# Performance work log

Measured on AMD Instinct MI355X. Metric: run time of the kernel, lower is better.

Reference implementation:

```python
import jax, jax.numpy as jnp
import numpy as np

DIM = 1024
NUM_HEADS = 16
HEAD_DIM = DIM // NUM_HEADS
SCALE = HEAD_DIM ** -0.5


def setup_inputs() -> dict:
    key = jax.random.key(0)
    ks = jax.random.split(key, 6)
    B, N, C = 2, 2048, DIM
    std = C ** -0.5
    return {
        "x_t": jax.random.normal(ks[0], (B, N, C), dtype=jnp.float32),
        "x_s": jax.random.normal(ks[1], (B, N, C), dtype=jnp.float32),
        "W_q": jax.random.normal(ks[2], (C, C), dtype=jnp.float32) * std,
        "W_kv": jax.random.normal(ks[3], (C, 2 * C), dtype=jnp.float32) * std,
        "W_fuse": jax.random.normal(ks[4], (C, C), dtype=jnp.float32) * std,
        "b_fuse": jax.random.normal(ks[5], (C,), dtype=jnp.float32) * 0.01,
    }


def reference(x_t, x_s, W_q, W_kv, W_fuse, b_fuse):
    B, N, C = x_t.shape
    H, D = NUM_HEADS, HEAD_DIM
    # q projection (no bias, qkv_bias=False): [B,N,C] -> [B,H,N,D]
    q = (x_t @ W_q).reshape(B, N, H, D).transpose(0, 2, 1, 3)
    # kv projection: [B,N,2C] -> k,v each [B,H,N,D]
    kv = (x_s @ W_kv).reshape(B, N, 2, H, D).transpose(2, 0, 3, 1, 4)
    k, v = kv[0], kv[1]
    # attention scores [B,H,N,N]
    attn = jnp.einsum("bhnd,bhmd->bhnm", q, k) * SCALE
    attn = jax.nn.softmax(attn, axis=-1)
    # weighted values -> [B,N,C]
    a = jnp.einsum("bhnm,bhmd->bhnd", attn, v).transpose(0, 2, 1, 3).reshape(B, N, C)
    # fuse projection (with bias); dropouts are identity (p=0)
    return a @ W_fuse + b_fuse
```

## Files before the change

### kernel.cpp

```cpp
#include <hip/hip_runtime.h>

#define SEQ 2048

typedef short short8 __attribute__((ext_vector_type(8)));
typedef float floatx4 __attribute__((ext_vector_type(4)));
typedef unsigned int uint2v __attribute__((ext_vector_type(2)));
typedef unsigned int uint4v __attribute__((ext_vector_type(4)));
typedef __fp16 f16x8 __attribute__((ext_vector_type(8)));

static __device__ __forceinline__ unsigned short f2bf(float f) {
    unsigned int u = __builtin_bit_cast(unsigned int, f);
    u = (u + 0x7fffu + ((u >> 16) & 1u)) >> 16;
    return (unsigned short)u;
}

#if __has_builtin(__builtin_amdgcn_cvt_pk_bf16_f32)
typedef __bf16 bf16x2 __attribute__((ext_vector_type(2)));
static __device__ __forceinline__ unsigned int pk_bf16(float a, float b) {
    bf16x2 v = __builtin_amdgcn_cvt_pk_bf16_f32(a, b);
    return __builtin_bit_cast(unsigned int, v);
}
#else
static __device__ __forceinline__ unsigned int pk_bf16(float a, float b) {
    return (unsigned int)f2bf(a) | ((unsigned int)f2bf(b) << 16);
}
#endif

static __device__ __forceinline__ unsigned int pk_f16(float a, float b) {
    auto v = __builtin_amdgcn_cvt_pkrtz(a, b);
    return __builtin_bit_cast(unsigned int, v);
}

#define GLD16(gp, lp)                                                        \
    __builtin_amdgcn_global_load_lds(                                        \
        (const __attribute__((address_space(1))) unsigned int*)(gp),         \
        (__attribute__((address_space(3))) unsigned int*)(lp), 16, 0, 0)

__global__ void prep_kernel(const float4* __restrict__ xa, const float4* __restrict__ xb,
                            ushort4* __restrict__ oa, ushort4* __restrict__ ob, float sa,
                            const float* __restrict__ Wq, const float* __restrict__ Wkv,
                            const float* __restrict__ Wf,
                            unsigned short* __restrict__ oq, unsigned short* __restrict__ okv,
                            unsigned short* __restrict__ of_) {
    __shared__ float tile[32][33];
    int bx = blockIdx.x, tid = threadIdx.x;
    if (bx < 8192) {
        int i = bx * 256 + tid;
        if (i < 1048576) {
            float4 v = xa[i];
            ushort4 o;
            o.x = f2bf(v.x * sa); o.y = f2bf(v.y * sa);
            o.z = f2bf(v.z * sa); o.w = f2bf(v.w * sa);
            oa[i] = o;
        } else {
            int j = i - 1048576;
            float4 v = xb[j];
            ushort4 o;
            o.x = f2bf(v.x); o.y = f2bf(v.y);
            o.z = f2bf(v.z); o.w = f2bf(v.w);
            ob[j] = o;
        }
        return;
    }
    int t2 = bx - 8192;
    const float* in; unsigned short* out; int N, t;
    if (t2 < 1024)      { in = Wq;  out = oq;  N = 1024; t = t2; }
    else if (t2 < 3072) { in = Wkv; out = okv; N = 2048; t = t2 - 1024; }
    else                { in = Wf;  out = of_; N = 1024; t = t2 - 3072; }
    int nb = N >> 5;
    int n0 = (t % nb) * 32, k0 = (t / nb) * 32;
    int tx = tid & 31, ty = tid >> 5;
#pragma unroll
    for (int i = 0; i < 4; i++)
        tile[ty + i * 8][tx] = in[(size_t)(k0 + ty + i * 8) * N + n0 + tx];
    __syncthreads();
#pragma unroll
    for (int i = 0; i < 4; i++)
        out[(size_t)(n0 + ty + i * 8) * 1024 + k0 + tx] = f2bf(tile[tx][ty + i * 8]);
}

__global__ __launch_bounds__(256, 3)
void gemm_qkv(const unsigned short* __restrict__ xt,
              const unsigned short* __restrict__ xs,
              const unsigned short* __restrict__ wq,
              const unsigned short* __restrict__ wkv,
              unsigned short* __restrict__ q_ws,
              unsigned short* __restrict__ k_ws,
              unsigned short* __restrict__ vt_ws) {
    __shared__ __align__(16) unsigned short smem_[16384];
    auto sA = (unsigned short(*)[64])smem_;
    auto sB = (unsigned short(*)[64])(smem_ + 8192);
    int tid = threadIdx.x, wave = tid >> 6, lane = tid & 63;
    int l15 = lane & 15, quad = lane >> 4;
    int cx = blockIdx.x;
    bool isq = cx < 8, isv = cx >= 16;
    const unsigned short* A  = isq ? xt : xs;
    const unsigned short* Bt = isq ? wq : wkv;
    int C0 = (isq ? cx : cx - 8) * 128;
    int R0 = blockIdx.y * 128;
    int wr = (wave >> 1) * 64, wc = (wave & 1) * 64;
    int srow = lane >> 3, scol = (lane & 7) * 8;

    floatx4 acc[4][4];
#pragma unroll
    for (int i = 0; i < 4; i++)
#pragma unroll
        for (int j = 0; j < 4; j++) acc[i][j] = (floatx4){0.f, 0.f, 0.f, 0.f};

    for (int kt = 0; kt < 16; kt++) {
        __syncthreads();
#pragma unroll
        for (int c = 0; c < 4; c++) {
            int rb = wave * 32 + c * 8;
            GLD16(&A [(size_t)(R0 + rb + srow) * 1024 + kt * 64 + scol], &sA[rb][0]);
            GLD16(&Bt[(size_t)(C0 + rb + srow) * 1024 + kt * 64 + scol], &sB[rb][0]);
        }
        __syncthreads();
#pragma unroll
        for (int ks = 0; ks < 2; ks++) {
            short8 af[4], bf[4];
#pragma unroll
            for (int mt = 0; mt < 4; mt++)
                af[mt] = *(const short8*)&sA[wr + mt * 16 + l15][ks * 32 + quad * 8];
#pragma unroll
            for (int nt = 0; nt < 4; nt++)
                bf[nt] = *(const short8*)&sB[wc + nt * 16 + l15][ks * 32 + quad * 8];
#pragma unroll
            for (int mt = 0; mt < 4; mt++)
#pragma unroll
                for (int nt = 0; nt < 4; nt++)
                    acc[mt][nt] = __builtin_amdgcn_mfma_f32_16x16x32_bf16(af[mt], bf[nt], acc[mt][nt], 0, 0, 0);
        }
    }

    int b = R0 >> 11, n0 = R0 & 2047;
    __syncthreads();

    if (!isv) {
#pragma unroll
        for (int mt = 0; mt < 4; mt++)
#pragma unroll
            for (int nt = 0; nt < 4; nt++) {
                int col = wc + nt * 16 + l15;
#pragma unroll
                for (int r = 0; r < 4; r++)
                    smem_[(wr + mt * 16 + quad * 4 + r) * 128 + col] = f2bf(acc[mt][nt][r]);
            }
        __syncthreads();
        unsigned short* out = isq ? q_ws : k_ws;
#pragma unroll
        for (int i = 0; i < 8; i++) {
            int u = tid + i * 256;
            int row = u >> 4, colg = u & 15;
            int n = n0 + row;
            int gc = C0 + colg * 8;
            int h = gc >> 6, d0 = gc & 63;
            int dd = isq ? d0 : ((((d0 >> 3) ^ (n & 7)) << 3));
            *(uint4v*)&out[((size_t)((b * 16 + h) * 2048 + n)) * 64 + dd] =
                *(const uint4v*)&smem_[row * 128 + colg * 8];
        }
    } else {
#pragma unroll
        for (int mt = 0; mt < 4; mt++)
#pragma unroll
            for (int nt = 0; nt < 4; nt++) {
                int cc = wc + nt * 16 + l15;
                int nl4 = (wr + mt * 16 + quad * 4) >> 2;
                int sw = nl4 ^ ((cc & 3) << 1);
                uint2v pk;
                pk.x = pk_f16(acc[mt][nt][0], acc[mt][nt][1]);
                pk.y = pk_f16(acc[mt][nt][2], acc[mt][nt][3]);
                *(uint2v*)&smem_[cc * 128 + (sw << 2)] = pk;
            }
        __syncthreads();
        int cb = C0 - 1024;
#pragma unroll
        for (int i = 0; i < 8; i++) {
            int u = tid + i * 256;
            int cc = u >> 4, ng = u & 15;
            int sw0 = (2 * ng) ^ ((cc & 3) << 1);
            uint4v val = *(const uint4v*)&smem_[cc * 128 + (sw0 << 2)];
            int ccv = cb + cc, h = ccv >> 6, d = ccv & 63;
            *(uint4v*)&vt_ws[((size_t)((b * 16 + h) * 64 + d)) * 2048 + n0 + ng * 8] = val;
        }
    }
}

__global__ __launch_bounds__(256, 3)
void gemm_fuse(const unsigned short* __restrict__ A,
               const unsigned short* __restrict__ Bt,
               float* __restrict__ out, const float* __restrict__ bias) {
    __shared__ unsigned short sA[128][64];
    __shared__ unsigned short sB[64][64];
    int tid = threadIdx.x, wave = tid >> 6, lane = tid & 63;
    int l15 = lane & 15, quad = lane >> 4;
    int R0 = blockIdx.y * 128, C0 = blockIdx.x * 64;
    int wr = (wave >> 1) * 64, wc = (wave & 1) * 32;
    int srow = lane >> 3, scol = (lane & 7) * 8;

    floatx4 acc[4][2];
#pragma unroll
    for (int i = 0; i < 4; i++)
#pragma unroll
        for (int j = 0; j < 2; j++) acc[i][j] = (floatx4){0.f, 0.f, 0.f, 0.f};

    for (int kt = 0; kt < 16; kt++) {
        __syncthreads();
#pragma unroll
        for (int c = 0; c < 4; c++) {
            int rb = wave * 32 + c * 8;
            GLD16(&A[(size_t)(R0 + rb + srow) * 1024 + kt * 64 + scol], &sA[rb][0]);
        }
#pragma unroll
        for (int c = 0; c < 2; c++) {
            int rb = wave * 16 + c * 8;
            GLD16(&Bt[(size_t)(C0 + rb + srow) * 1024 + kt * 64 + scol], &sB[rb][0]);
        }
        __syncthreads();
#pragma unroll
        for (int ks = 0; ks < 2; ks++) {
            short8 af[4], bf[2];
#pragma unroll
            for (int mt = 0; mt < 4; mt++)
                af[mt] = *(const short8*)&sA[wr + mt * 16 + l15][ks * 32 + quad * 8];
#pragma unroll
            for (int nt = 0; nt < 2; nt++)
                bf[nt] = *(const short8*)&sB[wc + nt * 16 + l15][ks * 32 + quad * 8];
#pragma unroll
            for (int mt = 0; mt < 4; mt++)
#pragma unroll
                for (int nt = 0; nt < 2; nt++)
                    acc[mt][nt] = __builtin_amdgcn_mfma_f32_16x16x32_bf16(af[mt], bf[nt], acc[mt][nt], 0, 0, 0);
        }
    }

#pragma unroll
    for (int mt = 0; mt < 4; mt++) {
#pragma unroll
        for (int r = 0; r < 4; r++) {
            int row = R0 + wr + mt * 16 + quad * 4 + r;
#pragma unroll
            for (int nt = 0; nt < 2; nt++) {
                int col = C0 + wc + nt * 16 + l15;
                out[(size_t)row * 1024 + col] = acc[mt][nt][r] + bias[col];
            }
        }
    }
}

__global__ __launch_bounds__(512, 4)
void attn_kernel(const unsigned short* __restrict__ Q,
                 const unsigned short* __restrict__ K,
                 const unsigned short* __restrict__ Vt,
                 unsigned short* __restrict__ Aout) {
    __shared__ __align__(16) unsigned short smem[32768];
    __shared__ float lred[8][2][16];

    int tid = threadIdx.x, wave = tid >> 6, lane = tid & 63;
    int l15 = lane & 15, quad = lane >> 4;
    int kq = wave & 3;
    int g  = wave >> 2;

    int id = blockIdx.x;
    int logical = (id & 7) * 128 + (id >> 3);
    int bh = logical >> 5, qt = logical & 31;
    int b = bh >> 4, h = bh & 15;
    int qr0 = qt * 64 + g * 32;

    const unsigned short* Qp = Q + (size_t)bh * SEQ * 64;
    const unsigned short* Kp = K + (size_t)bh * SEQ * 64;
    const unsigned short* Vp = Vt + (size_t)bh * 64 * SEQ;

    int srow = lane >> 3, scol = (lane & 7) * 8;
    int vscol = scol ^ (srow << 3);
    int wk0 = kq * 16;

#define STAGE(t, kb)                                                          \
    {                                                                         \
        GLD16(&Kp[(size_t)((t) * 64 + wave * 8 + srow) * 64 + scol],          \
              &smem[(kb) + wave * 8 * 64]);                                   \
        GLD16(&Vp[(size_t)(wave * 8 + srow) * 2048 + (t) * 64 + vscol],       \
              &smem[16384 + (kb) + wave * 8 * 64]);                           \
    }

    short8 qf[2][2];
#pragma unroll
    for (int nt = 0; nt < 2; nt++)
#pragma unroll
        for (int ks = 0; ks < 2; ks++)
            qf[nt][ks] = *(const short8*)&Qp[(size_t)(qr0 + nt * 16 + l15) * 64 + ks * 32 + quad * 8];

    STAGE(0, 0) STAGE(1, 4096) STAGE(2, 8192) STAGE(3, 12288)

    floatx4 of[4][2];
#pragma unroll
    for (int i = 0; i < 4; i++)
#pragma unroll
        for (int j = 0; j < 2; j++) of[i][j] = (floatx4){0.f, 0.f, 0.f, 0.f};
    floatx4 of_l[2];
#pragma unroll
    for (int i = 0; i < 2; i++) of_l[i] = (floatx4){0.f, 0.f, 0.f, 0.f};

    f16x8 vones;
#pragma unroll
    for (int i = 0; i < 8; i++) vones[i] = (__fp16)1.0f;

    int krow = wk0 + l15;
    int ksw = (l15 & 7) << 3;
    int kaddr0 = krow * 64 + ((quad * 8) ^ ksw);
    int kaddr1 = krow * 64 + ((32 + quad * 8) ^ ksw);
    int vcol = (wk0 + quad * 4) ^ ksw;

    asm volatile("s_waitcnt vmcnt(0)" ::: "memory");
    __syncthreads();

    auto compute_pair = [&](int kb) {
        __builtin_amdgcn_s_setprio(1);
        uint2v pka[2], pkb[2];
        {
            short8 kf0 = *(const short8*)&smem[kb + kaddr0];
            short8 kf1 = *(const short8*)&smem[kb + kaddr1];
#pragma unroll
            for (int nt = 0; nt < 2; nt++) {
                floatx4 z = (floatx4){0.f, 0.f, 0.f, 0.f};
                floatx4 s = __builtin_amdgcn_mfma_f32_16x16x32_bf16(kf0, qf[nt][0], z, 0, 0, 0);
                s = __builtin_amdgcn_mfma_f32_16x16x32_bf16(kf1, qf[nt][1], s, 0, 0, 0);
                pka[nt].x = pk_f16(__builtin_amdgcn_exp2f(s[0]), __builtin_amdgcn_exp2f(s[1]));
                pka[nt].y = pk_f16(__builtin_amdgcn_exp2f(s[2]), __builtin_amdgcn_exp2f(s[3]));
            }
        }
        {
            short8 kf0 = *(const short8*)&smem[kb + 4096 + kaddr0];
            short8 kf1 = *(const short8*)&smem[kb + 4096 + kaddr1];
#pragma unroll
            for (int nt = 0; nt < 2; nt++) {
                floatx4 z = (floatx4){0.f, 0.f, 0.f, 0.f};
                floatx4 s = __builtin_amdgcn_mfma_f32_16x16x32_bf16(kf0, qf[nt][0], z, 0, 0, 0);
                s = __builtin_amdgcn_mfma_f32_16x16x32_bf16(kf1, qf[nt][1], s, 0, 0, 0);
                pkb[nt].x = pk_f16(__builtin_amdgcn_exp2f(s[0]), __builtin_amdgcn_exp2f(s[1]));
                pkb[nt].y = pk_f16(__builtin_amdgcn_exp2f(s[2]), __builtin_amdgcn_exp2f(s[3]));
            }
        }
#pragma unroll
        for (int dt = 0; dt < 4; dt++) {
            int vbase = 16384 + kb + (dt * 16 + l15) * 64 + vcol;
            uint2v va = *(const uint2v*)&smem[vbase];
            uint2v vb = *(const uint2v*)&smem[vbase + 4096];
            f16x8 vf = __builtin_bit_cast(f16x8, (uint4v){va.x, va.y, vb.x, vb.y});
#pragma unroll
            for (int nt = 0; nt < 2; nt++) {
                f16x8 pf = __builtin_bit_cast(f16x8, (uint4v){pka[nt].x, pka[nt].y, pkb[nt].x, pkb[nt].y});
                of[dt][nt] = __builtin_amdgcn_mfma_f32_16x16x32_f16(vf, pf, of[dt][nt], 0, 0, 0);
            }
        }
#pragma unroll
        for (int nt = 0; nt < 2; nt++) {
            f16x8 pf = __builtin_bit_cast(f16x8, (uint4v){pka[nt].x, pka[nt].y, pkb[nt].x, pkb[nt].y});
            of_l[nt] = __builtin_amdgcn_mfma_f32_16x16x32_f16(vones, pf, of_l[nt], 0, 0, 0);
        }
        __builtin_amdgcn_s_setprio(0);
    };

#pragma unroll 2
    for (int p = 0; p < 14; p++) {
        int kb = (p & 1) * 8192;
        compute_pair(kb);
        __builtin_amdgcn_sched_barrier(0);
        asm volatile("s_barrier" ::: "memory");
        STAGE(2 * p + 4, kb)
        STAGE(2 * p + 5, kb + 4096)
        asm volatile("s_waitcnt vmcnt(4)" ::: "memory");
        asm volatile("s_barrier" ::: "memory");
        __builtin_amdgcn_sched_barrier(0);
    }
    compute_pair(0);
    asm volatile("s_waitcnt vmcnt(0)" ::: "memory");
    asm volatile("s_barrier" ::: "memory");
    compute_pair(8192);
#undef STAGE

    if (quad == 0) {
#pragma unroll
        for (int nt = 0; nt < 2; nt++) lred[wave][nt][l15] = of_l[nt][0];
    }
    __syncthreads();

    float* red = (float*)smem;

#pragma unroll
    for (int dt = 0; dt < 4; dt++)
#pragma unroll
        for (int nt = 0; nt < 2; nt++)
            *(floatx4*)&red[(wave * 8 + dt * 2 + nt) * 256 + lane * 4] = of[dt][nt];
    __syncthreads();

    {
        int mydt = kq;
#pragma unroll
        for (int nt = 0; nt < 2; nt++) {
            floatx4 s = *(const floatx4*)&red[((g * 4 + 0) * 8 + mydt * 2 + nt) * 256 + lane * 4];
#pragma unroll
            for (int wg = 1; wg < 4; wg++)
                s += *(const floatx4*)&red[((g * 4 + wg) * 8 + mydt * 2 + nt) * 256 + lane * 4];
            float lt = lred[g * 4 + 0][nt][l15] + lred[g * 4 + 1][nt][l15] +
                       lred[g * 4 + 2][nt][l15] + lred[g * 4 + 3][nt][l15];
            float inv = 1.f / lt;
            int row = qr0 + nt * 16 + l15;
            uint2v o;
            o.x = pk_bf16(s[0] * inv, s[1] * inv);
            o.y = pk_bf16(s[2] * inv, s[3] * inv);
            *(uint2v*)&Aout[(size_t)(b * SEQ + row) * 1024 + h * 64 + mydt * 16 + quad * 4] = o;
        }
    }
}

extern "C" void kernel_launch(void* const* d_in, const int* in_sizes, int n_in,
                              void* d_out, int out_size, void* d_ws, size_t ws_size,
                              hipStream_t stream) {
    const float* x_t  = (const float*)d_in[0];
    const float* x_s  = (const float*)d_in[1];
    const float* W_q  = (const float*)d_in[2];
    const float* W_kv = (const float*)d_in[3];
    const float* W_f  = (const float*)d_in[4];
    const float* b_f  = (const float*)d_in[5];
    float* out = (float*)d_out;

    char* ws = (char*)d_ws;
    const size_t MB = 1u << 20;
    unsigned short* xt_bf = (unsigned short*)(ws);
    unsigned short* xs_bf = (unsigned short*)(ws + 8 * MB);
    unsigned short* wq_t  = (unsigned short*)(ws + 16 * MB);
    unsigned short* wkv_t = (unsigned short*)(ws + 18 * MB);
    unsigned short* wf_t  = (unsigned short*)(ws + 22 * MB);
    unsigned short* q_ws  = (unsigned short*)(ws + 24 * MB);
    unsigned short* k_ws  = (unsigned short*)(ws + 32 * MB);
    unsigned short* vt_ws = (unsigned short*)(ws + 40 * MB);
    unsigned short* a_ws  = (unsigned short*)(ws + 48 * MB);

    prep_kernel<<<12288, 256, 0, stream>>>((const float4*)x_t, (const float4*)x_s,
                                           (ushort4*)xt_bf, (ushort4*)xs_bf,
                                           0.125f * 1.44269504088896340736f,
                                           W_q, W_kv, W_f, wq_t, wkv_t, wf_t);

    gemm_qkv<<<dim3(24, 32), 256, 0, stream>>>(xt_bf, xs_bf, wq_t, wkv_t, q_ws, k_ws, vt_ws);
    attn_kernel<<<1024, 512, 0, stream>>>(q_ws, k_ws, vt_ws, a_ws);
    gemm_fuse<<<dim3(16, 32), 256, 0, stream>>>(a_ws, wf_t, out, b_f);
}
```

Measured before the change: 195.3 us.

## Double query rows per attention block to halve K/V reloads

Each attention block now handles 128 query rows instead of 64, so each wave computes 4 query sub-tiles against every staged K/V tile, and the grid shrinks from 1024 to 512 blocks. This halves the global and LDS traffic for K and V per query row and raises MFMA work per staged tile. The cross-wave reduction is split into two passes over LDS to fit the larger accumulators. In exchange, register pressure roughly doubles for the accumulators and Q fragments, and fewer blocks may leave some compute units underused.

```diff
diff --git a/kernel.cpp b/kernel.cpp
--- a/kernel.cpp
+++ b/kernel.cpp
@@ -254,7 +254,7 @@
                  const unsigned short* __restrict__ Vt,
                  unsigned short* __restrict__ Aout) {
     __shared__ __align__(16) unsigned short smem[32768];
-    __shared__ float lred[8][2][16];
+    __shared__ float lred[8][4][16];
 
     int tid = threadIdx.x, wave = tid >> 6, lane = tid & 63;
     int l15 = lane & 15, quad = lane >> 4;
@@ -262,10 +262,10 @@
     int g  = wave >> 2;
 
     int id = blockIdx.x;
-    int logical = (id & 7) * 128 + (id >> 3);
-    int bh = logical >> 5, qt = logical & 31;
+    int logical = (id & 7) * 64 + (id >> 3);
+    int bh = logical >> 4, qt = logical & 15;
     int b = bh >> 4, h = bh & 15;
-    int qr0 = qt * 64 + g * 32;
+    int qr0 = qt * 128 + g * 64;
 
     const unsigned short* Qp = Q + (size_t)bh * SEQ * 64;
     const unsigned short* Kp = K + (size_t)bh * SEQ * 64;
@@ -283,23 +283,23 @@
               &smem[16384 + (kb) + wave * 8 * 64]);                           \
     }
 
-    short8 qf[2][2];
-#pragma unroll
-    for (int nt = 0; nt < 2; nt++)
+    short8 qf[4][2];
+#pragma unroll
+    for (int nt = 0; nt < 4; nt++)
 #pragma unroll
         for (int ks = 0; ks < 2; ks++)
             qf[nt][ks] = *(const short8*)&Qp[(size_t)(qr0 + nt * 16 + l15) * 64 + ks * 32 + quad * 8];
 
     STAGE(0, 0) STAGE(1, 4096) STAGE(2, 8192) STAGE(3, 12288)
 
-    floatx4 of[4][2];
+    floatx4 of[4][4];
 #pragma unroll
     for (int i = 0; i < 4; i++)
 #pragma unroll
-        for (int j = 0; j < 2; j++) of[i][j] = (floatx4){0.f, 0.f, 0.f, 0.f};
-    floatx4 of_l[2];
-#pragma unroll
-    for (int i = 0; i < 2; i++) of_l[i] = (floatx4){0.f, 0.f, 0.f, 0.f};
+        for (int j = 0; j < 4; j++) of[i][j] = (floatx4){0.f, 0.f, 0.f, 0.f};
+    floatx4 of_l[4];
+#pragma unroll
+    for (int i = 0; i < 4; i++) of_l[i] = (floatx4){0.f, 0.f, 0.f, 0.f};
 
     f16x8 vones;
 #pragma unroll
@@ -316,12 +316,12 @@
 
     auto compute_pair = [&](int kb) {
         __builtin_amdgcn_s_setprio(1);
-        uint2v pka[2], pkb[2];
+        uint2v pka[4], pkb[4];
         {
             short8 kf0 = *(const short8*)&smem[kb + kaddr0];
             short8 kf1 = *(const short8*)&smem[kb + kaddr1];
 #pragma unroll
-            for (int nt = 0; nt < 2; nt++) {
+            for (int nt = 0; nt < 4; nt++) {
                 floatx4 z = (floatx4){0.f, 0.f, 0.f, 0.f};
                 floatx4 s = __builtin_amdgcn_mfma_f32_16x16x32_bf16(kf0, qf[nt][0], z, 0, 0, 0);
                 s = __builtin_amdgcn_mfma_f32_16x16x32_bf16(kf1, qf[nt][1], s, 0, 0, 0);
@@ -333,7 +333,7 @@
             short8 kf0 = *(const short8*)&smem[kb + 4096 + kaddr0];
             short8 kf1 = *(const short8*)&smem[kb + 4096 + kaddr1];
 #pragma unroll
-            for (int nt = 0; nt < 2; nt++) {
+            for (int nt = 0; nt < 4; nt++) {
                 floatx4 z = (floatx4){0.f, 0.f, 0.f, 0.f};
                 floatx4 s = __builtin_amdgcn_mfma_f32_16x16x32_bf16(kf0, qf[nt][0], z, 0, 0, 0);
                 s = __builtin_amdgcn_mfma_f32_16x16x32_bf16(kf1, qf[nt][1], s, 0, 0, 0);
@@ -348,13 +348,13 @@
             uint2v vb = *(const uint2v*)&smem[vbase + 4096];
             f16x8 vf = __builtin_bit_cast(f16x8, (uint4v){va.x, va.y, vb.x, vb.y});
 #pragma unroll
-            for (int nt = 0; nt < 2; nt++) {
+            for (int nt = 0; nt < 4; nt++) {
                 f16x8 pf = __builtin_bit_cast(f16x8, (uint4v){pka[nt].x, pka[nt].y, pkb[nt].x, pkb[nt].y});
                 of[dt][nt] = __builtin_amdgcn_mfma_f32_16x16x32_f16(vf, pf, of[dt][nt], 0, 0, 0);
             }
         }
 #pragma unroll
-        for (int nt = 0; nt < 2; nt++) {
+        for (int nt = 0; nt < 4; nt++) {
             f16x8 pf = __builtin_bit_cast(f16x8, (uint4v){pka[nt].x, pka[nt].y, pkb[nt].x, pkb[nt].y});
             of_l[nt] = __builtin_amdgcn_mfma_f32_16x16x32_f16(vones, pf, of_l[nt], 0, 0, 0);
         }
@@ -381,36 +381,55 @@
 
     if (quad == 0) {
 #pragma unroll
-        for (int nt = 0; nt < 2; nt++) lred[wave][nt][l15] = of_l[nt][0];
+        for (int nt = 0; nt < 4; nt++) lred[wave][nt][l15] = of_l[nt][0];
     }
     __syncthreads();
 
     float* red = (float*)smem;
-
-#pragma unroll
-    for (int dt = 0; dt < 4; dt++)
-#pragma unroll
-        for (int nt = 0; nt < 2; nt++)
-            *(floatx4*)&red[(wave * 8 + dt * 2 + nt) * 256 + lane * 4] = of[dt][nt];
-    __syncthreads();
-
-    {
-        int mydt = kq;
-#pragma unroll
-        for (int nt = 0; nt < 2; nt++) {
-            floatx4 s = *(const floatx4*)&red[((g * 4 + 0) * 8 + mydt * 2 + nt) * 256 + lane * 4];
-#pragma unroll
-            for (int wg = 1; wg < 4; wg++)
-                s += *(const floatx4*)&red[((g * 4 + wg) * 8 + mydt * 2 + nt) * 256 + lane * 4];
-            float lt = lred[g * 4 + 0][nt][l15] + lred[g * 4 + 1][nt][l15] +
-                       lred[g * 4 + 2][nt][l15] + lred[g * 4 + 3][nt][l15];
-            float inv = 1.f / lt;
-            int row = qr0 + nt * 16 + l15;
-            uint2v o;
-            o.x = pk_bf16(s[0] * inv, s[1] * inv);
-            o.y = pk_bf16(s[2] * inv, s[3] * inv);
-            *(uint2v*)&Aout[(size_t)(b * SEQ + row) * 1024 + h * 64 + mydt * 16 + quad * 4] = o;
-        }
+    int myc = kq >> 1, nt0 = (kq & 1) * 2;
+
+#pragma unroll
+    for (int nt = 0; nt < 4; nt++) {
+        *(floatx4*)&red[((0 * 2 + g) * 4 + kq) * 1024 + nt * 256 + lane * 4] = of[0][nt];
+        *(floatx4*)&red[((1 * 2 + g) * 4 + kq) * 1024 + nt * 256 + lane * 4] = of[1][nt];
+    }
+    __syncthreads();
+#pragma unroll
+    for (int j = 0; j < 2; j++) {
+        int nt = nt0 + j;
+        floatx4 s = (floatx4){0.f, 0.f, 0.f, 0.f};
+#pragma unroll
+        for (int k4 = 0; k4 < 4; k4++)
+            s += *(const floatx4*)&red[((myc * 2 + g) * 4 + k4) * 1024 + nt * 256 + lane * 4];
+        float lt = lred[g * 4 + 0][nt][l15] + lred[g * 4 + 1][nt][l15] +
+                   lred[g * 4 + 2][nt][l15] + lred[g * 4 + 3][nt][l15];
+        float inv = 1.f / lt;
+        uint2v o;
+        o.x = pk_bf16(s[0] * inv, s[1] * inv);
+        o.y = pk_bf16(s[2] * inv, s[3] * inv);
+        *(uint2v*)&Aout[(size_t)(b * SEQ + qr0 + nt * 16 + l15) * 1024 + h * 64 + myc * 16 + quad * 4] = o;
+    }
+    __syncthreads();
+#pragma unroll
+    for (int nt = 0; nt < 4; nt++) {
+        *(floatx4*)&red[((0 * 2 + g) * 4 + kq) * 1024 + nt * 256 + lane * 4] = of[2][nt];
+        *(floatx4*)&red[((1 * 2 + g) * 4 + kq) * 1024 + nt * 256 + lane * 4] = of[3][nt];
+    }
+    __syncthreads();
+#pragma unroll
+    for (int j = 0; j < 2; j++) {
+        int nt = nt0 + j;
+        floatx4 s = (floatx4){0.f, 0.f, 0.f, 0.f};
+#pragma unroll
+        for (int k4 = 0; k4 < 4; k4++)
+            s += *(const floatx4*)&red[((myc * 2 + g) * 4 + k4) * 1024 + nt * 256 + lane * 4];
+        float lt = lred[g * 4 + 0][nt][l15] + lred[g * 4 + 1][nt][l15] +
+                   lred[g * 4 + 2][nt][l15] + lred[g * 4 + 3][nt][l15];
+        float inv = 1.f / lt;
+        uint2v o;
+        o.x = pk_bf16(s[0] * inv, s[1] * inv);
+        o.y = pk_bf16(s[2] * inv, s[3] * inv);
+        *(uint2v*)&Aout[(size_t)(b * SEQ + qr0 + nt * 16 + l15) * 1024 + h * 64 + (myc + 2) * 16 + quad * 4] = o;
     }
 }
 
@@ -443,6 +462,6 @@
                                            W_q, W_kv, W_f, wq_t, wkv_t, wf_t);
 
     gemm_qkv<<<dim3(24, 32), 256, 0, stream>>>(xt_bf, xs_bf, wq_t, wkv_t, q_ws, k_ws, vt_ws);
-    attn_kernel<<<1024, 512, 0, stream>>>(q_ws, k_ws, vt_ws, a_ws);
+    attn_kernel<<<512, 512, 0, stream>>>(q_ws, k_ws, vt_ws, a_ws);
     gemm_fuse<<<dim3(16, 32), 256, 0, stream>>>(a_ws, wf_t, out, b_f);
 }
```

After: 364.5 us. 1.87x slower.

## Widen attention query tile to 128 rows with 2-way key split per row group

Applied to the files above, without the earlier changes.

The attention kernel now handles 128 query rows per block instead of 64, with 4 row groups of 2 waves each splitting the keys, rather than 2 groups of 4 waves. Each staged K/V tile is reused by twice as many query rows, which halves the global K/V traffic and the number of blocks launched. The cross-wave reduction shrinks from 4 partials to 2. In exchange only 512 blocks are launched, which gives less parallelism across CUs and may leave the machine partly idle.

```diff
diff --git a/kernel.cpp b/kernel.cpp
--- a/kernel.cpp
+++ b/kernel.cpp
@@ -258,14 +258,14 @@
 
     int tid = threadIdx.x, wave = tid >> 6, lane = tid & 63;
     int l15 = lane & 15, quad = lane >> 4;
-    int kq = wave & 3;
-    int g  = wave >> 2;
+    int g  = wave >> 1;
+    int kh = wave & 1;
 
     int id = blockIdx.x;
-    int logical = (id & 7) * 128 + (id >> 3);
-    int bh = logical >> 5, qt = logical & 31;
+    int logical = (id & 7) * 64 + (id >> 3);
+    int bh = logical >> 4, qt = logical & 15;
     int b = bh >> 4, h = bh & 15;
-    int qr0 = qt * 64 + g * 32;
+    int qr0 = qt * 128 + g * 32;
 
     const unsigned short* Qp = Q + (size_t)bh * SEQ * 64;
     const unsigned short* Kp = K + (size_t)bh * SEQ * 64;
@@ -273,7 +273,7 @@
 
     int srow = lane >> 3, scol = (lane & 7) * 8;
     int vscol = scol ^ (srow << 3);
-    int wk0 = kq * 16;
+    int wk0 = kh * 32;
 
 #define STAGE(t, kb)                                                          \
     {                                                                         \
@@ -305,59 +305,65 @@
 #pragma unroll
     for (int i = 0; i < 8; i++) vones[i] = (__fp16)1.0f;
 
-    int krow = wk0 + l15;
     int ksw = (l15 & 7) << 3;
-    int kaddr0 = krow * 64 + ((quad * 8) ^ ksw);
-    int kaddr1 = krow * 64 + ((32 + quad * 8) ^ ksw);
-    int vcol = (wk0 + quad * 4) ^ ksw;
+    int ka0 = (wk0 + l15) * 64 + ((quad * 8) ^ ksw);
+    int ka1 = (wk0 + l15) * 64 + ((32 + quad * 8) ^ ksw);
+    int ka2 = (wk0 + 16 + l15) * 64 + ((quad * 8) ^ ksw);
+    int ka3 = (wk0 + 16 + l15) * 64 + ((32 + quad * 8) ^ ksw);
+    int vcol0 = (wk0 + quad * 4) ^ ksw;
+    int vcol1 = (wk0 + 16 + quad * 4) ^ ksw;
 
     asm volatile("s_waitcnt vmcnt(0)" ::: "memory");
     __syncthreads();
 
-    auto compute_pair = [&](int kb) {
-        __builtin_amdgcn_s_setprio(1);
-        uint2v pka[2], pkb[2];
+    auto compute_tile = [&](int tb) {
+        uint2v p0[2], p1[2];
         {
-            short8 kf0 = *(const short8*)&smem[kb + kaddr0];
-            short8 kf1 = *(const short8*)&smem[kb + kaddr1];
+            short8 kf0 = *(const short8*)&smem[tb + ka0];
+            short8 kf1 = *(const short8*)&smem[tb + ka1];
 #pragma unroll
             for (int nt = 0; nt < 2; nt++) {
                 floatx4 z = (floatx4){0.f, 0.f, 0.f, 0.f};
                 floatx4 s = __builtin_amdgcn_mfma_f32_16x16x32_bf16(kf0, qf[nt][0], z, 0, 0, 0);
                 s = __builtin_amdgcn_mfma_f32_16x16x32_bf16(kf1, qf[nt][1], s, 0, 0, 0);
-                pka[nt].x = pk_f16(__builtin_amdgcn_exp2f(s[0]), __builtin_amdgcn_exp2f(s[1]));
-                pka[nt].y = pk_f16(__builtin_amdgcn_exp2f(s[2]), __builtin_amdgcn_exp2f(s[3]));
+                p0[nt].x = pk_f16(__builtin_amdgcn_exp2f(s[0]), __builtin_amdgcn_exp2f(s[1]));
+                p0[nt].y = pk_f16(__builtin_amdgcn_exp2f(s[2]), __builtin_amdgcn_exp2f(s[3]));
             }
         }
         {
-            short8 kf0 = *(const short8*)&smem[kb + 4096 + kaddr0];
-            short8 kf1 = *(const short8*)&smem[kb + 4096 + kaddr1];
+            short8 kf0 = *(const short8*)&smem[tb + ka2];
+            short8 kf1 = *(const short8*)&smem[tb + ka3];
 #pragma unroll
             for (int nt = 0; nt < 2; nt++) {
                 floatx4 z = (floatx4){0.f, 0.f, 0.f, 0.f};
                 floatx4 s = __builtin_amdgcn_mfma_f32_16x16x32_bf16(kf0, qf[nt][0], z, 0, 0, 0);
                 s = __builtin_amdgcn_mfma_f32_16x16x32_bf16(kf1, qf[nt][1], s, 0, 0, 0);
-                pkb[nt].x = pk_f16(__builtin_amdgcn_exp2f(s[0]), __builtin_amdgcn_exp2f(s[1]));
-                pkb[nt].y = pk_f16(__builtin_amdgcn_exp2f(s[2]), __builtin_amdgcn_exp2f(s[3]));
+                p1[nt].x = pk_f16(__builtin_amdgcn_exp2f(s[0]), __builtin_amdgcn_exp2f(s[1]));
+                p1[nt].y = pk_f16(__builtin_amdgcn_exp2f(s[2]), __builtin_amdgcn_exp2f(s[3]));
             }
         }
 #pragma unroll
         for (int dt = 0; dt < 4; dt++) {
-            int vbase = 16384 + kb + (dt * 16 + l15) * 64 + vcol;
-            uint2v va = *(const uint2v*)&smem[vbase];
-            uint2v vb = *(const uint2v*)&smem[vbase + 4096];
+            int vbase = 16384 + tb + (dt * 16 + l15) * 64;
+            uint2v va = *(const uint2v*)&smem[vbase + vcol0];
+            uint2v vb = *(const uint2v*)&smem[vbase + vcol1];
             f16x8 vf = __builtin_bit_cast(f16x8, (uint4v){va.x, va.y, vb.x, vb.y});
 #pragma unroll
             for (int nt = 0; nt < 2; nt++) {
-                f16x8 pf = __builtin_bit_cast(f16x8, (uint4v){pka[nt].x, pka[nt].y, pkb[nt].x, pkb[nt].y});
+                f16x8 pf = __builtin_bit_cast(f16x8, (uint4v){p0[nt].x, p0[nt].y, p1[nt].x, p1[nt].y});
                 of[dt][nt] = __builtin_amdgcn_mfma_f32_16x16x32_f16(vf, pf, of[dt][nt], 0, 0, 0);
             }
         }
 #pragma unroll
         for (int nt = 0; nt < 2; nt++) {
-            f16x8 pf = __builtin_bit_cast(f16x8, (uint4v){pka[nt].x, pka[nt].y, pkb[nt].x, pkb[nt].y});
+            f16x8 pf = __builtin_bit_cast(f16x8, (uint4v){p0[nt].x, p0[nt].y, p1[nt].x, p1[nt].y});
             of_l[nt] = __builtin_amdgcn_mfma_f32_16x16x32_f16(vones, pf, of_l[nt], 0, 0, 0);
         }
+    };
+    auto compute_pair = [&](int kb) {
+        __builtin_amdgcn_s_setprio(1);
+        compute_tile(kb);
+        compute_tile(kb + 4096);
         __builtin_amdgcn_s_setprio(0);
     };
 
@@ -391,25 +397,22 @@
     for (int dt = 0; dt < 4; dt++)
 #pragma unroll
         for (int nt = 0; nt < 2; nt++)
-            *(floatx4*)&red[(wave * 8 + dt * 2 + nt) * 256 + lane * 4] = of[dt][nt];
+            *(floatx4*)&red[((wave * 4 + dt) * 2 + nt) * 256 + lane * 4] = of[dt][nt];
     __syncthreads();
 
-    {
-        int mydt = kq;
+#pragma unroll
+    for (int dd = 0; dd < 2; dd++) {
+        int dt = kh * 2 + dd;
 #pragma unroll
         for (int nt = 0; nt < 2; nt++) {
-            floatx4 s = *(const floatx4*)&red[((g * 4 + 0) * 8 + mydt * 2 + nt) * 256 + lane * 4];
-#pragma unroll
-            for (int wg = 1; wg < 4; wg++)
-                s += *(const floatx4*)&red[((g * 4 + wg) * 8 + mydt * 2 + nt) * 256 + lane * 4];
-            float lt = lred[g * 4 + 0][nt][l15] + lred[g * 4 + 1][nt][l15] +
-                       lred[g * 4 + 2][nt][l15] + lred[g * 4 + 3][nt][l15];
+            floatx4 s = *(const floatx4*)&red[(((g * 2 + 0) * 4 + dt) * 2 + nt) * 256 + lane * 4]
+                      + *(const floatx4*)&red[(((g * 2 + 1) * 4 + dt) * 2 + nt) * 256 + lane * 4];
+            float lt = lred[g * 2 + 0][nt][l15] + lred[g * 2 + 1][nt][l15];
             float inv = 1.f / lt;
-            int row = qr0 + nt * 16 + l15;
             uint2v o;
             o.x = pk_bf16(s[0] * inv, s[1] * inv);
             o.y = pk_bf16(s[2] * inv, s[3] * inv);
-            *(uint2v*)&Aout[(size_t)(b * SEQ + row) * 1024 + h * 64 + mydt * 16 + quad * 4] = o;
+            *(uint2v*)&Aout[(size_t)(b * SEQ + qr0 + nt * 16 + l15) * 1024 + h * 64 + dt * 16 + quad * 4] = o;
         }
     }
 }
@@ -443,6 +446,6 @@
                                            W_q, W_kv, W_f, wq_t, wkv_t, wf_t);
 
     gemm_qkv<<<dim3(24, 32), 256, 0, stream>>>(xt_bf, xs_bf, wq_t, wkv_t, q_ws, k_ws, vt_ws);
-    attn_kernel<<<1024, 512, 0, stream>>>(q_ws, k_ws, vt_ws, a_ws);
+    attn_kernel<<<512, 512, 0, stream>>>(q_ws, k_ws, vt_ws, a_ws);
     gemm_fuse<<<dim3(16, 32), 256, 0, stream>>>(a_ws, wf_t, out, b_f);
 }
```

New measurement: 191.1 us. 2.1% less time.
